# Kernel optimization log

Measured on AMD Instinct MI355X. Metric: run time of the kernel, lower is better.

The kernel has to match this reference:

```python
import jax, jax.numpy as jnp
import numpy as np

B, T, N, IN, H, P = 1, 48, 4096, 2, 64, 12


def _normalize_adj(adj):
    A = adj + jnp.eye(adj.shape[0], dtype=adj.dtype)
    d = jnp.sum(A, axis=1)
    dinv = jnp.where(d > 0, d ** -0.5, 0.0)
    return (dinv[:, None] * A) * dinv[None, :]


def _cell(inp, h, c, A, gcWi, gcbi, gcWh, gcbh, liWi, libi, liWh, libh):
    # graph conv: spmm(A, inp @ W) + bias, plus plain linears; all produce [BN, 4H]
    comb = (A @ (inp @ gcWi) + gcbi
            + A @ (h @ gcWh) + gcbh
            + inp @ liWi + libi
            + h @ liWh + libh)
    i_g, f_g, o_g, g_g = jnp.split(comb, 4, axis=1)
    new_c = jax.nn.sigmoid(f_g) * c + jax.nn.sigmoid(i_g) * jnp.tanh(g_g)
    new_h = jax.nn.sigmoid(o_g) * jnp.tanh(new_c)
    return new_h, new_c


def setup_inputs() -> dict:
    key = jax.random.key(0)
    ks = jax.random.split(key, 24)
    s_in = 1.0 / np.sqrt(4 * H)

    def p(k, shape):
        return jax.random.normal(k, shape, dtype=jnp.float32) * s_in

    adj = (jax.random.uniform(ks[1], (N, N)) < 0.01).astype(jnp.float32)
    return {
        "x": jax.random.normal(ks[0], (B, T, N * IN), dtype=jnp.float32),
        "adj": adj,
        "gcWi0": p(ks[2], (IN, 4 * H)), "gcbi0": p(ks[3], (4 * H,)),
        "gcWh0": p(ks[4], (H, 4 * H)), "gcbh0": p(ks[5], (4 * H,)),
        "liWi0": p(ks[6], (IN, 4 * H)), "libi0": p(ks[7], (4 * H,)),
        "liWh0": p(ks[8], (H, 4 * H)), "libh0": p(ks[9], (4 * H,)),
        "gcWi1": p(ks[10], (H, 4 * H)), "gcbi1": p(ks[11], (4 * H,)),
        "gcWh1": p(ks[12], (H, 4 * H)), "gcbh1": p(ks[13], (4 * H,)),
        "liWi1": p(ks[14], (H, 4 * H)), "libi1": p(ks[15], (4 * H,)),
        "liWh1": p(ks[16], (H, 4 * H)), "libh1": p(ks[17], (4 * H,)),
        "outW": p(ks[18], (H, P)), "outb": p(ks[19], (P,)),
    }


def reference(x, adj, gcWi0, gcbi0, gcWh0, gcbh0, liWi0, libi0, liWh0, libh0,
              gcWi1, gcbi1, gcWh1, gcbh1, liWi1, libi1, liWh1, libh1, outW, outb):
    A = _normalize_adj(adj)
    # [B,T,N*IN] -> time-major [T, B*N, IN]
    xs = x.reshape(B, T, N, IN).transpose(1, 0, 2, 3).reshape(T, B * N, IN)
    z = jnp.zeros((B * N, H), dtype=x.dtype)

    def step(carry, xt):
        h0, c0, h1, c1 = carry
        h0, c0 = _cell(xt, h0, c0, A, gcWi0, gcbi0, gcWh0, gcbh0,
                       liWi0, libi0, liWh0, libh0)
        # dropout is identity in eval mode
        h1, c1 = _cell(h0, h1, c1, A, gcWi1, gcbi1, gcWh1, gcbh1,
                       liWi1, libi1, liWh1, libh1)
        return (h0, c0, h1, c1), None

    (h0, c0, h1, c1), _ = jax.lax.scan(step, (z, z, z, z), xs)
    out = h1 @ outW + outb  # [B*N, P]
    return out.reshape(B, N, P)
```

## Files before the change

### kernel.cpp

```cpp
#include <hip/hip_runtime.h>
#include <math.h>

#define NN 4096
#define TT 48
#define HH 64
#define GG 256
#define PP 12
#define CAP 192
#define NH (NN * HH)

__device__ __forceinline__ float bcast_f(float v, int lane) {
  return __int_as_float(__builtin_amdgcn_readlane(__float_as_int(v), lane));
}
__device__ __forceinline__ int bcast_i(int v, int lane) {
  return __builtin_amdgcn_readlane(v, lane);
}

__launch_bounds__(256)
__global__ void k_prep(const float* gcbi0, const float* gcbh0,
                       const float* libi0, const float* libh0,
                       const float* gcbi1, const float* gcbh1,
                       const float* libi1, const float* libh1,
                       const float* gcWh0, const float* liWh0,
                       const float* gcWi1, const float* liWi1,
                       const float* gcWh1, const float* liWh1,
                       const float* gcWi0, const float* liWi0,
                       float* state, float4* Wg0, float4* Wg1,
                       float4* biasg0, float4* biasg1, float4* xq0) {
  int idx = blockIdx.x * 256 + threadIdx.x;
  int stride = gridDim.x * 256;
  for (int i = idx; i < 6 * NH; i += stride) state[i] = 0.0f;
  for (int i = idx; i < 64 * 2 * 64; i += stride) {
    int j = i & 63, m = (i >> 6) & 1, k = i >> 7;
    const float* W = m ? liWh0 : gcWh0;
    Wg0[i] = make_float4(W[k * GG + j], W[k * GG + j + 64],
                         W[k * GG + j + 128], W[k * GG + j + 192]);
  }
  for (int i = idx; i < 64 * 4 * 64; i += stride) {
    int j = i & 63, m = (i >> 6) & 3, k = i >> 8;
    const float* W = (m == 0) ? gcWi1 : (m == 1) ? liWi1 : (m == 2) ? gcWh1 : liWh1;
    Wg1[i] = make_float4(W[k * GG + j], W[k * GG + j + 64],
                         W[k * GG + j + 128], W[k * GG + j + 192]);
  }
  if (idx < 64) {
    int j = idx;
    biasg0[j] = make_float4(
        gcbi0[j] + gcbh0[j] + libi0[j] + libh0[j],
        gcbi0[j + 64] + gcbh0[j + 64] + libi0[j + 64] + libh0[j + 64],
        gcbi0[j + 128] + gcbh0[j + 128] + libi0[j + 128] + libh0[j + 128],
        gcbi0[j + 192] + gcbh0[j + 192] + libi0[j + 192] + libh0[j + 192]);
    biasg1[j] = make_float4(
        gcbi1[j] + gcbh1[j] + libi1[j] + libh1[j],
        gcbi1[j + 64] + gcbh1[j + 64] + libi1[j + 64] + libh1[j + 64],
        gcbi1[j + 128] + gcbh1[j + 128] + libi1[j + 128] + libh1[j + 128],
        gcbi1[j + 192] + gcbh1[j + 192] + libi1[j + 192] + libh1[j + 192]);
  } else if (idx < 320) {
    int i = idx - 64;
    int j = i & 63, m = i >> 6;
    const float* W = (m < 2) ? gcWi0 : liWi0;
    int kk = m & 1;
    xq0[i] = make_float4(W[kk * GG + j], W[kk * GG + j + 64],
                         W[kk * GG + j + 128], W[kk * GG + j + 192]);
  }
}

__launch_bounds__(256)
__global__ void k_build(const float* adj, float* dinv,
                        int* ell_col, float* ell_val, int* ell_cnt) {
  int r = blockIdx.x;
  __shared__ int cnt;
  __shared__ float red[256];
  if (threadIdx.x == 0) cnt = 0;
  __syncthreads();
  const float* row = adj + (size_t)r * NN;
  float s = 0.0f;
  for (int c = threadIdx.x; c < NN; c += 256) {
    float a = row[c];
    if (c == r) a += 1.0f;
    s += a;
    if (a != 0.0f) {
      int pos = atomicAdd(&cnt, 1);
      if (pos < CAP) {
        ell_col[(size_t)r * CAP + pos] = c;
        ell_val[(size_t)r * CAP + pos] = a;
      }
    }
  }
  red[threadIdx.x] = s;
  __syncthreads();
  for (int st = 128; st > 0; st >>= 1) {
    if (threadIdx.x < st) red[threadIdx.x] += red[threadIdx.x + st];
    __syncthreads();
  }
  int n = cnt < CAP ? cnt : CAP;
  for (int j = n + (int)threadIdx.x; j < CAP; j += 256) {
    ell_col[(size_t)r * CAP + j] = 0;
    ell_val[(size_t)r * CAP + j] = 0.0f;
  }
  if (threadIdx.x == 0) {
    int npad = (n + 7) & ~7;
    if (npad > CAP) npad = CAP;
    ell_cnt[r] = npad;
    dinv[r] = 1.0f / sqrtf(red[0]);
  }
}

__launch_bounds__(256)
__global__ void k_scale(const float* dinv, const int* ell_col, float* ell_val) {
  int idx = blockIdx.x * 256 + threadIdx.x;
  int r = idx / CAP;
  if (r >= NN) return;
  float v = ell_val[idx];
  if (v != 0.0f) ell_val[idx] = v * dinv[r] * dinv[ell_col[idx]];
}

__launch_bounds__(256)
__global__ void k_gax(const float* x, const int* ell_col, const float* ell_val,
                      const int* ell_cnt, float* gax) {
  int t = blockIdx.x >> 3;
  int seg = blockIdx.x & 7;
  __shared__ float xs[NN * 2];
  const float* xt = x + (size_t)t * NN * 2;
  for (int i = threadIdx.x; i < NN * 2; i += 256) xs[i] = xt[i];
  __syncthreads();
  int base = seg * 512 * 2;
  for (int oo = threadIdx.x; oo < 512 * 2; oo += 256) {
    int o = base + oo;
    int r = o >> 1, cmp = o & 1;
    int cnt = ell_cnt[r];
    const int* cp = ell_col + (size_t)r * CAP;
    const float* vp = ell_val + (size_t)r * CAP;
    float acc = 0.0f;
    for (int j = 0; j < cnt; j += 4) {
      acc += vp[j]     * xs[cp[j]     * 2 + cmp];
      acc += vp[j + 1] * xs[cp[j + 1] * 2 + cmp];
      acc += vp[j + 2] * xs[cp[j + 2] * 2 + cmp];
      acc += vp[j + 3] * xs[cp[j + 3] * 2 + cmp];
    }
    gax[(size_t)t * NN * 2 + o] = acc;
  }
}

__device__ __forceinline__ void cell0_body(
    int blk,
    const int* __restrict__ ell_col, const float* __restrict__ ell_val,
    const int* __restrict__ ell_cnt,
    const float2* __restrict__ Pr, float* __restrict__ Pw,
    float* __restrict__ c0,
    const float* __restrict__ xt, const float* __restrict__ gaxt,
    const float4* __restrict__ Wg0, const float4* __restrict__ biasg0,
    const float4* __restrict__ xq0) {
  const int tid = threadIdx.x;
  const int wave = tid >> 6, lane = tid & 63;
  const int r0 = blk * 8 + wave * 2;

  int myc[2][3]; float myv[2][3]; int cnts[2];
#pragma unroll
  for (int rr = 0; rr < 2; rr++) {
    int r = r0 + rr;
    cnts[rr] = ell_cnt[r];
#pragma unroll
    for (int chk = 0; chk < 3; chk++) {
      myc[rr][chk] = ell_col[(size_t)r * CAP + chk * 64 + lane];
      myv[rr][chk] = ell_val[(size_t)r * CAP + chk * 64 + lane];
    }
  }
  float gacc[2], hl[2];
#pragma unroll
  for (int rr = 0; rr < 2; rr++) {
    int cnt = cnts[rr];
    float acc = 0.0f;
#pragma unroll
    for (int chk = 0; chk < 3; chk++) {
      int base = chk * 64;
      if (base < cnt) {
        int lim = cnt - base; if (lim > 64) lim = 64;
        int mc = myc[rr][chk]; float mv = myv[rr][chk];
        for (int m = 0; m < lim; m += 8) {
          float2 ld[8]; float vv[8];
#pragma unroll
          for (int i = 0; i < 8; i++) {
            int cc = bcast_i(mc, m + i);
            vv[i] = bcast_f(mv, m + i);
            ld[i] = Pr[(size_t)cc * 64 + lane];
          }
#pragma unroll
          for (int i = 0; i < 8; i++) acc += vv[i] * ld[i].x;
        }
      }
    }
    gacc[rr] = acc;
    hl[rr] = Pr[(size_t)(r0 + rr) * 64 + lane].x;
  }

  float4 acc[2];
  {
    float4 b = biasg0[lane];
    float4 qg0 = xq0[lane], qg1 = xq0[64 + lane];
    float4 ql0 = xq0[128 + lane], ql1 = xq0[192 + lane];
#pragma unroll
    for (int rr = 0; rr < 2; rr++) {
      float xx0 = xt[(size_t)(r0 + rr) * 2];
      float xx1 = xt[(size_t)(r0 + rr) * 2 + 1];
      float gg0 = gaxt[(size_t)(r0 + rr) * 2];
      float gg1 = gaxt[(size_t)(r0 + rr) * 2 + 1];
      acc[rr].x = b.x + gg0 * qg0.x + gg1 * qg1.x + xx0 * ql0.x + xx1 * ql1.x;
      acc[rr].y = b.y + gg0 * qg0.y + gg1 * qg1.y + xx0 * ql0.y + xx1 * ql1.y;
      acc[rr].z = b.z + gg0 * qg0.z + gg1 * qg1.z + xx0 * ql0.z + xx1 * ql1.z;
      acc[rr].w = b.w + gg0 * qg0.w + gg1 * qg1.w + xx0 * ql0.w + xx1 * ql1.w;
    }
  }

  const float4* bw = Wg0 + lane;
#pragma unroll 4
  for (int k = 0; k < 64; k++) {
    float4 w0 = bw[(k * 2 + 0) * 64];
    float4 w1 = bw[(k * 2 + 1) * 64];
#pragma unroll
    for (int rr = 0; rr < 2; rr++) {
      float a0 = bcast_f(gacc[rr], k);
      float a1 = bcast_f(hl[rr], k);
      acc[rr].x += a0 * w0.x + a1 * w1.x;
      acc[rr].y += a0 * w0.y + a1 * w1.y;
      acc[rr].z += a0 * w0.z + a1 * w1.z;
      acc[rr].w += a0 * w0.w + a1 * w1.w;
    }
  }

#pragma unroll
  for (int rr = 0; rr < 2; rr++) {
    size_t gi = (size_t)(r0 + rr) * HH + lane;
    float cprev = c0[gi];
    float si = 1.0f / (1.0f + __expf(-acc[rr].x));
    float sf = 1.0f / (1.0f + __expf(-acc[rr].y));
    float so = 1.0f / (1.0f + __expf(-acc[rr].z));
    float cn = sf * cprev + si * tanhf(acc[rr].w);
    float hn = so * tanhf(cn);
    c0[gi] = cn;
    Pw[gi * 2 + 0] = hn;
  }
}

__device__ __forceinline__ void cell1_body(
    int blk,
    const int* __restrict__ ell_col, const float* __restrict__ ell_val,
    const int* __restrict__ ell_cnt,
    const float2* __restrict__ Pr, float* __restrict__ Pw,
    float* __restrict__ c1,
    const float4* __restrict__ Wg1, const float4* __restrict__ biasg1) {
  const int tid = threadIdx.x;
  const int wave = tid >> 6, lane = tid & 63;
  const int r0 = blk * 8 + wave * 2;

  int myc[2][3]; float myv[2][3]; int cnts[2];
#pragma unroll
  for (int rr = 0; rr < 2; rr++) {
    int r = r0 + rr;
    cnts[rr] = ell_cnt[r];
#pragma unroll
    for (int chk = 0; chk < 3; chk++) {
      myc[rr][chk] = ell_col[(size_t)r * CAP + chk * 64 + lane];
      myv[rr][chk] = ell_val[(size_t)r * CAP + chk * 64 + lane];
    }
  }
  float ga0[2], ga1[2], hl0[2], hl1[2];
#pragma unroll
  for (int rr = 0; rr < 2; rr++) {
    int cnt = cnts[rr];
    float a0 = 0.0f, a1 = 0.0f;
#pragma unroll
    for (int chk = 0; chk < 3; chk++) {
      int base = chk * 64;
      if (base < cnt) {
        int lim = cnt - base; if (lim > 64) lim = 64;
        int mc = myc[rr][chk]; float mv = myv[rr][chk];
        for (int m = 0; m < lim; m += 8) {
          float2 ld[8]; float vv[8];
#pragma unroll
          for (int i = 0; i < 8; i++) {
            int cc = bcast_i(mc, m + i);
            vv[i] = bcast_f(mv, m + i);
            ld[i] = Pr[(size_t)cc * 64 + lane];
          }
#pragma unroll
          for (int i = 0; i < 8; i++) {
            a0 += vv[i] * ld[i].x;
            a1 += vv[i] * ld[i].y;
          }
        }
      }
    }
    ga0[rr] = a0;
    ga1[rr] = a1;
    float2 hh = Pr[(size_t)(r0 + rr) * 64 + lane];
    hl0[rr] = hh.x;
    hl1[rr] = hh.y;
  }

  float4 acc[2];
  {
    float4 b = biasg1[lane];
    acc[0] = b; acc[1] = b;
  }
  const float4* bw = Wg1 + lane;
#pragma unroll 4
  for (int k = 0; k < 64; k++) {
    float4 w0 = bw[(k * 4 + 0) * 64];
    float4 w1 = bw[(k * 4 + 1) * 64];
    float4 w2 = bw[(k * 4 + 2) * 64];
    float4 w3 = bw[(k * 4 + 3) * 64];
#pragma unroll
    for (int rr = 0; rr < 2; rr++) {
      float a0 = bcast_f(ga0[rr], k);
      float a1 = bcast_f(hl0[rr], k);
      float a2 = bcast_f(ga1[rr], k);
      float a3 = bcast_f(hl1[rr], k);
      acc[rr].x += a0 * w0.x + a1 * w1.x + a2 * w2.x + a3 * w3.x;
      acc[rr].y += a0 * w0.y + a1 * w1.y + a2 * w2.y + a3 * w3.y;
      acc[rr].z += a0 * w0.z + a1 * w1.z + a2 * w2.z + a3 * w3.z;
      acc[rr].w += a0 * w0.w + a1 * w1.w + a2 * w2.w + a3 * w3.w;
    }
  }

#pragma unroll
  for (int rr = 0; rr < 2; rr++) {
    size_t gi = (size_t)(r0 + rr) * HH + lane;
    float cprev = c1[gi];
    float si = 1.0f / (1.0f + __expf(-acc[rr].x));
    float sf = 1.0f / (1.0f + __expf(-acc[rr].y));
    float so = 1.0f / (1.0f + __expf(-acc[rr].z));
    float cn = sf * cprev + si * tanhf(acc[rr].w);
    float hn = so * tanhf(cn);
    c1[gi] = cn;
    Pw[gi * 2 + 1] = hn;
  }
}

__launch_bounds__(256)
__global__ void k_cells(int c0blocks,
                        const int* __restrict__ ell_col,
                        const float* __restrict__ ell_val,
                        const int* __restrict__ ell_cnt,
                        const float2* __restrict__ Pr, float* __restrict__ Pw,
                        float* __restrict__ c0, float* __restrict__ c1,
                        const float* __restrict__ xt, const float* __restrict__ gaxt,
                        const float4* __restrict__ Wg0,
                        const float4* __restrict__ biasg0,
                        const float4* __restrict__ xq0,
                        const float4* __restrict__ Wg1,
                        const float4* __restrict__ biasg1) {
  int b = blockIdx.x;
  if (b < c0blocks) {
    cell0_body(b, ell_col, ell_val, ell_cnt, Pr, Pw, c0, xt, gaxt,
               Wg0, biasg0, xq0);
  } else {
    cell1_body(b - c0blocks, ell_col, ell_val, ell_cnt, Pr, Pw, c1,
               Wg1, biasg1);
  }
}

__launch_bounds__(256)
__global__ void k_out(const float* __restrict__ P0, const float* __restrict__ outW,
                      const float* __restrict__ outb, float* __restrict__ out) {
  int idx = blockIdx.x * 256 + threadIdx.x;
  if (idx >= NN * PP) return;
  int r = idx / PP, p = idx - r * PP;
  float acc = outb[p];
  const float* hrow = P0 + (size_t)r * 128;
#pragma unroll 16
  for (int k = 0; k < HH; k++) acc += hrow[k * 2 + 1] * outW[k * PP + p];
  out[idx] = acc;
}

extern "C" void kernel_launch(void* const* d_in, const int* in_sizes, int n_in,
                              void* d_out, int out_size, void* d_ws, size_t ws_size,
                              hipStream_t stream) {
  const float* x     = (const float*)d_in[0];
  const float* adj   = (const float*)d_in[1];
  const float* gcWi0 = (const float*)d_in[2];
  const float* gcbi0 = (const float*)d_in[3];
  const float* gcWh0 = (const float*)d_in[4];
  const float* gcbh0 = (const float*)d_in[5];
  const float* liWi0 = (const float*)d_in[6];
  const float* libi0 = (const float*)d_in[7];
  const float* liWh0 = (const float*)d_in[8];
  const float* libh0 = (const float*)d_in[9];
  const float* gcWi1 = (const float*)d_in[10];
  const float* gcbi1 = (const float*)d_in[11];
  const float* gcWh1 = (const float*)d_in[12];
  const float* gcbh1 = (const float*)d_in[13];
  const float* liWi1 = (const float*)d_in[14];
  const float* libi1 = (const float*)d_in[15];
  const float* liWh1 = (const float*)d_in[16];
  const float* libh1 = (const float*)d_in[17];
  const float* outW  = (const float*)d_in[18];
  const float* outb  = (const float*)d_in[19];

  char* ws = (char*)d_ws;
  size_t off = 0;
  auto carve = [&](size_t bytes) {
    void* p = ws + off;
    off += (bytes + 255) & ~(size_t)255;
    return p;
  };
  float*  dinv    = (float*)carve((size_t)NN * 4);
  int*    ell_col = (int*)carve((size_t)NN * CAP * 4);
  float*  ell_val = (float*)carve((size_t)NN * CAP * 4);
  int*    ell_cnt = (int*)carve((size_t)NN * 4);
  float*  state   = (float*)carve((size_t)6 * NH * 4);
  float*  gax     = (float*)carve((size_t)TT * NN * 2 * 4);
  float4* Wg0     = (float4*)carve((size_t)64 * 2 * 64 * 16);
  float4* Wg1     = (float4*)carve((size_t)64 * 4 * 64 * 16);
  float4* biasg0  = (float4*)carve((size_t)64 * 16);
  float4* biasg1  = (float4*)carve((size_t)64 * 16);
  float4* xq0     = (float4*)carve((size_t)256 * 16);

  float* P[2] = {state, state + 2 * NH};
  float* c0 = state + 4 * NH;
  float* c1 = state + 5 * NH;

  k_prep<<<512, 256, 0, stream>>>(gcbi0, gcbh0, libi0, libh0,
                                  gcbi1, gcbh1, libi1, libh1,
                                  gcWh0, liWh0, gcWi1, liWi1, gcWh1, liWh1,
                                  gcWi0, liWi0,
                                  state, Wg0, Wg1, biasg0, biasg1, xq0);
  k_build<<<NN, 256, 0, stream>>>(adj, dinv, ell_col, ell_val, ell_cnt);
  k_scale<<<(NN * CAP) / 256, 256, 0, stream>>>(dinv, ell_col, ell_val);
  k_gax<<<TT * 8, 256, 0, stream>>>(x, ell_col, ell_val, ell_cnt, gax);

  for (int k = 0; k <= TT; k++) {
    int A = k & 1;
    int c0blocks = (k < TT) ? NN / 8 : 0;
    int c1blocks = (k > 0) ? NN / 8 : 0;
    int grid = c0blocks + c1blocks;
    int tx = (k < TT) ? k : (TT - 1);
    k_cells<<<grid, 256, 0, stream>>>(
        c0blocks, ell_col, ell_val, ell_cnt,
        (const float2*)P[A ^ 1], P[A], c0, c1,
        x + (size_t)tx * NN * 2, gax + (size_t)tx * NN * 2,
        Wg0, biasg0, xq0, Wg1, biasg1);
  }

  k_out<<<(NN * PP + 255) / 256, 256, 0, stream>>>(P[0], outW, outb, (float*)d_out);
}
```

Before: 2.080 ms.

## Split dense gate matmul across waves by K-slices with shared-memory reduction

Each block now stages its 8 rows of aggregated activations and hidden state in shared memory. Each wave then handles a 16-wide K slice for all 8 rows instead of the full K range for 2 rows, so every wave loads only a quarter of the weight matrix per block. Partial sums are reduced through shared memory by wave 0, which then applies the LSTM gates. This cuts redundant weight loads, at the cost of two block barriers, about 30KB of LDS per block, a serialized epilogue on one wave, and a launch bound hint of 4 blocks per CU.

```diff
diff --git a/kernel.cpp b/kernel.cpp
--- a/kernel.cpp
+++ b/kernel.cpp
@@ -141,8 +141,10 @@
   }
 }
 
+#define ASTR 65
+
 __device__ __forceinline__ void cell0_body(
-    int blk,
+    int blk, float* actS, float4* redS,
     const int* __restrict__ ell_col, const float* __restrict__ ell_val,
     const int* __restrict__ ell_cnt,
     const float2* __restrict__ Pr, float* __restrict__ Pw,
@@ -152,30 +154,21 @@
     const float4* __restrict__ xq0) {
   const int tid = threadIdx.x;
   const int wave = tid >> 6, lane = tid & 63;
-  const int r0 = blk * 8 + wave * 2;
-
-  int myc[2][3]; float myv[2][3]; int cnts[2];
+  const int r0 = blk * 8;
+
 #pragma unroll
   for (int rr = 0; rr < 2; rr++) {
-    int r = r0 + rr;
-    cnts[rr] = ell_cnt[r];
-#pragma unroll
-    for (int chk = 0; chk < 3; chk++) {
-      myc[rr][chk] = ell_col[(size_t)r * CAP + chk * 64 + lane];
-      myv[rr][chk] = ell_val[(size_t)r * CAP + chk * 64 + lane];
-    }
-  }
-  float gacc[2], hl[2];
-#pragma unroll
-  for (int rr = 0; rr < 2; rr++) {
-    int cnt = cnts[rr];
+    int rloc = 2 * wave + rr;
+    int r = r0 + rloc;
+    int cnt = ell_cnt[r];
     float acc = 0.0f;
 #pragma unroll
     for (int chk = 0; chk < 3; chk++) {
       int base = chk * 64;
       if (base < cnt) {
         int lim = cnt - base; if (lim > 64) lim = 64;
-        int mc = myc[rr][chk]; float mv = myv[rr][chk];
+        int mc = ell_col[(size_t)r * CAP + base + lane];
+        float mv = ell_val[(size_t)r * CAP + base + lane];
         for (int m = 0; m < lim; m += 8) {
           float2 ld[8]; float vv[8];
 #pragma unroll
@@ -189,60 +182,86 @@
         }
       }
     }
-    gacc[rr] = acc;
-    hl[rr] = Pr[(size_t)(r0 + rr) * 64 + lane].x;
-  }
-
-  float4 acc[2];
-  {
+    actS[(rloc * 2 + 0) * ASTR + lane] = acc;
+    actS[(rloc * 2 + 1) * ASTR + lane] = Pr[(size_t)r * 64 + lane].x;
+  }
+  __syncthreads();
+
+  const int kk0 = wave * 16;
+  const int lm = lane & 1, lk = (lane >> 1) & 15;
+  float areg[8];
+#pragma unroll
+  for (int r = 0; r < 8; r++)
+    areg[r] = actS[(r * 2 + lm) * ASTR + kk0 + lk];
+
+  float4 acc[8];
+  if (wave == 0) {
     float4 b = biasg0[lane];
     float4 qg0 = xq0[lane], qg1 = xq0[64 + lane];
     float4 ql0 = xq0[128 + lane], ql1 = xq0[192 + lane];
 #pragma unroll
-    for (int rr = 0; rr < 2; rr++) {
-      float xx0 = xt[(size_t)(r0 + rr) * 2];
-      float xx1 = xt[(size_t)(r0 + rr) * 2 + 1];
-      float gg0 = gaxt[(size_t)(r0 + rr) * 2];
-      float gg1 = gaxt[(size_t)(r0 + rr) * 2 + 1];
-      acc[rr].x = b.x + gg0 * qg0.x + gg1 * qg1.x + xx0 * ql0.x + xx1 * ql1.x;
-      acc[rr].y = b.y + gg0 * qg0.y + gg1 * qg1.y + xx0 * ql0.y + xx1 * ql1.y;
-      acc[rr].z = b.z + gg0 * qg0.z + gg1 * qg1.z + xx0 * ql0.z + xx1 * ql1.z;
-      acc[rr].w = b.w + gg0 * qg0.w + gg1 * qg1.w + xx0 * ql0.w + xx1 * ql1.w;
-    }
+    for (int r = 0; r < 8; r++) {
+      float xx0 = xt[(size_t)(r0 + r) * 2];
+      float xx1 = xt[(size_t)(r0 + r) * 2 + 1];
+      float gg0 = gaxt[(size_t)(r0 + r) * 2];
+      float gg1 = gaxt[(size_t)(r0 + r) * 2 + 1];
+      acc[r].x = b.x + gg0 * qg0.x + gg1 * qg1.x + xx0 * ql0.x + xx1 * ql1.x;
+      acc[r].y = b.y + gg0 * qg0.y + gg1 * qg1.y + xx0 * ql0.y + xx1 * ql1.y;
+      acc[r].z = b.z + gg0 * qg0.z + gg1 * qg1.z + xx0 * ql0.z + xx1 * ql1.z;
+      acc[r].w = b.w + gg0 * qg0.w + gg1 * qg1.w + xx0 * ql0.w + xx1 * ql1.w;
+    }
+  } else {
+#pragma unroll
+    for (int r = 0; r < 8; r++) acc[r] = make_float4(0.f, 0.f, 0.f, 0.f);
   }
 
   const float4* bw = Wg0 + lane;
-#pragma unroll 4
-  for (int k = 0; k < 64; k++) {
+#pragma unroll
+  for (int kk = 0; kk < 16; kk++) {
+    int k = kk0 + kk;
     float4 w0 = bw[(k * 2 + 0) * 64];
     float4 w1 = bw[(k * 2 + 1) * 64];
 #pragma unroll
-    for (int rr = 0; rr < 2; rr++) {
-      float a0 = bcast_f(gacc[rr], k);
-      float a1 = bcast_f(hl[rr], k);
-      acc[rr].x += a0 * w0.x + a1 * w1.x;
-      acc[rr].y += a0 * w0.y + a1 * w1.y;
-      acc[rr].z += a0 * w0.z + a1 * w1.z;
-      acc[rr].w += a0 * w0.w + a1 * w1.w;
-    }
-  }
-
-#pragma unroll
-  for (int rr = 0; rr < 2; rr++) {
-    size_t gi = (size_t)(r0 + rr) * HH + lane;
-    float cprev = c0[gi];
-    float si = 1.0f / (1.0f + __expf(-acc[rr].x));
-    float sf = 1.0f / (1.0f + __expf(-acc[rr].y));
-    float so = 1.0f / (1.0f + __expf(-acc[rr].z));
-    float cn = sf * cprev + si * tanhf(acc[rr].w);
-    float hn = so * tanhf(cn);
-    c0[gi] = cn;
-    Pw[gi * 2 + 0] = hn;
+    for (int r = 0; r < 8; r++) {
+      float a0 = bcast_f(areg[r], kk * 2 + 0);
+      float a1 = bcast_f(areg[r], kk * 2 + 1);
+      acc[r].x += a0 * w0.x + a1 * w1.x;
+      acc[r].y += a0 * w0.y + a1 * w1.y;
+      acc[r].z += a0 * w0.z + a1 * w1.z;
+      acc[r].w += a0 * w0.w + a1 * w1.w;
+    }
+  }
+
+  if (wave > 0) {
+#pragma unroll
+    for (int r = 0; r < 8; r++)
+      redS[(wave - 1) * 512 + r * 64 + lane] = acc[r];
+  }
+  __syncthreads();
+  if (wave == 0) {
+#pragma unroll
+    for (int r = 0; r < 8; r++) {
+      float4 t = acc[r];
+#pragma unroll
+      for (int w = 0; w < 3; w++) {
+        float4 p = redS[w * 512 + r * 64 + lane];
+        t.x += p.x; t.y += p.y; t.z += p.z; t.w += p.w;
+      }
+      size_t gi = (size_t)(r0 + r) * HH + lane;
+      float cprev = c0[gi];
+      float si = 1.0f / (1.0f + __expf(-t.x));
+      float sf = 1.0f / (1.0f + __expf(-t.y));
+      float so = 1.0f / (1.0f + __expf(-t.z));
+      float cn = sf * cprev + si * tanhf(t.w);
+      float hn = so * tanhf(cn);
+      c0[gi] = cn;
+      Pw[gi * 2 + 0] = hn;
+    }
   }
 }
 
 __device__ __forceinline__ void cell1_body(
-    int blk,
+    int blk, float* actS, float4* redS,
     const int* __restrict__ ell_col, const float* __restrict__ ell_val,
     const int* __restrict__ ell_cnt,
     const float2* __restrict__ Pr, float* __restrict__ Pw,
@@ -250,30 +269,21 @@
     const float4* __restrict__ Wg1, const float4* __restrict__ biasg1) {
   const int tid = threadIdx.x;
   const int wave = tid >> 6, lane = tid & 63;
-  const int r0 = blk * 8 + wave * 2;
-
-  int myc[2][3]; float myv[2][3]; int cnts[2];
+  const int r0 = blk * 8;
+
 #pragma unroll
   for (int rr = 0; rr < 2; rr++) {
-    int r = r0 + rr;
-    cnts[rr] = ell_cnt[r];
-#pragma unroll
-    for (int chk = 0; chk < 3; chk++) {
-      myc[rr][chk] = ell_col[(size_t)r * CAP + chk * 64 + lane];
-      myv[rr][chk] = ell_val[(size_t)r * CAP + chk * 64 + lane];
-    }
-  }
-  float ga0[2], ga1[2], hl0[2], hl1[2];
-#pragma unroll
-  for (int rr = 0; rr < 2; rr++) {
-    int cnt = cnts[rr];
+    int rloc = 2 * wave + rr;
+    int r = r0 + rloc;
+    int cnt = ell_cnt[r];
     float a0 = 0.0f, a1 = 0.0f;
 #pragma unroll
     for (int chk = 0; chk < 3; chk++) {
       int base = chk * 64;
       if (base < cnt) {
         int lim = cnt - base; if (lim > 64) lim = 64;
-        int mc = myc[rr][chk]; float mv = myv[rr][chk];
+        int mc = ell_col[(size_t)r * CAP + base + lane];
+        float mv = ell_val[(size_t)r * CAP + base + lane];
         for (int m = 0; m < lim; m += 8) {
           float2 ld[8]; float vv[8];
 #pragma unroll
@@ -290,53 +300,81 @@
         }
       }
     }
-    ga0[rr] = a0;
-    ga1[rr] = a1;
-    float2 hh = Pr[(size_t)(r0 + rr) * 64 + lane];
-    hl0[rr] = hh.x;
-    hl1[rr] = hh.y;
-  }
-
-  float4 acc[2];
-  {
+    float2 hh = Pr[(size_t)r * 64 + lane];
+    actS[(rloc * 4 + 0) * ASTR + lane] = a0;
+    actS[(rloc * 4 + 1) * ASTR + lane] = hh.x;
+    actS[(rloc * 4 + 2) * ASTR + lane] = a1;
+    actS[(rloc * 4 + 3) * ASTR + lane] = hh.y;
+  }
+  __syncthreads();
+
+  const int kk0 = wave * 16;
+  const int lm = lane & 3, lk = lane >> 2;
+  float areg[8];
+#pragma unroll
+  for (int r = 0; r < 8; r++)
+    areg[r] = actS[(r * 4 + lm) * ASTR + kk0 + lk];
+
+  float4 acc[8];
+  if (wave == 0) {
     float4 b = biasg1[lane];
-    acc[0] = b; acc[1] = b;
-  }
+#pragma unroll
+    for (int r = 0; r < 8; r++) acc[r] = b;
+  } else {
+#pragma unroll
+    for (int r = 0; r < 8; r++) acc[r] = make_float4(0.f, 0.f, 0.f, 0.f);
+  }
+
   const float4* bw = Wg1 + lane;
-#pragma unroll 4
-  for (int k = 0; k < 64; k++) {
+#pragma unroll
+  for (int kk = 0; kk < 16; kk++) {
+    int k = kk0 + kk;
     float4 w0 = bw[(k * 4 + 0) * 64];
     float4 w1 = bw[(k * 4 + 1) * 64];
     float4 w2 = bw[(k * 4 + 2) * 64];
     float4 w3 = bw[(k * 4 + 3) * 64];
 #pragma unroll
-    for (int rr = 0; rr < 2; rr++) {
-      float a0 = bcast_f(ga0[rr], k);
-      float a1 = bcast_f(hl0[rr], k);
-      float a2 = bcast_f(ga1[rr], k);
-      float a3 = bcast_f(hl1[rr], k);
-      acc[rr].x += a0 * w0.x + a1 * w1.x + a2 * w2.x + a3 * w3.x;
-      acc[rr].y += a0 * w0.y + a1 * w1.y + a2 * w2.y + a3 * w3.y;
-      acc[rr].z += a0 * w0.z + a1 * w1.z + a2 * w2.z + a3 * w3.z;
-      acc[rr].w += a0 * w0.w + a1 * w1.w + a2 * w2.w + a3 * w3.w;
-    }
-  }
-
-#pragma unroll
-  for (int rr = 0; rr < 2; rr++) {
-    size_t gi = (size_t)(r0 + rr) * HH + lane;
-    float cprev = c1[gi];
-    float si = 1.0f / (1.0f + __expf(-acc[rr].x));
-    float sf = 1.0f / (1.0f + __expf(-acc[rr].y));
-    float so = 1.0f / (1.0f + __expf(-acc[rr].z));
-    float cn = sf * cprev + si * tanhf(acc[rr].w);
-    float hn = so * tanhf(cn);
-    c1[gi] = cn;
-    Pw[gi * 2 + 1] = hn;
-  }
-}
-
-__launch_bounds__(256)
+    for (int r = 0; r < 8; r++) {
+      float a0 = bcast_f(areg[r], kk * 4 + 0);
+      float a1 = bcast_f(areg[r], kk * 4 + 1);
+      float a2 = bcast_f(areg[r], kk * 4 + 2);
+      float a3 = bcast_f(areg[r], kk * 4 + 3);
+      acc[r].x += a0 * w0.x + a1 * w1.x + a2 * w2.x + a3 * w3.x;
+      acc[r].y += a0 * w0.y + a1 * w1.y + a2 * w2.y + a3 * w3.y;
+      acc[r].z += a0 * w0.z + a1 * w1.z + a2 * w2.z + a3 * w3.z;
+      acc[r].w += a0 * w0.w + a1 * w1.w + a2 * w2.w + a3 * w3.w;
+    }
+  }
+
+  if (wave > 0) {
+#pragma unroll
+    for (int r = 0; r < 8; r++)
+      redS[(wave - 1) * 512 + r * 64 + lane] = acc[r];
+  }
+  __syncthreads();
+  if (wave == 0) {
+#pragma unroll
+    for (int r = 0; r < 8; r++) {
+      float4 t = acc[r];
+#pragma unroll
+      for (int w = 0; w < 3; w++) {
+        float4 p = redS[w * 512 + r * 64 + lane];
+        t.x += p.x; t.y += p.y; t.z += p.z; t.w += p.w;
+      }
+      size_t gi = (size_t)(r0 + r) * HH + lane;
+      float cprev = c1[gi];
+      float si = 1.0f / (1.0f + __expf(-t.x));
+      float sf = 1.0f / (1.0f + __expf(-t.y));
+      float so = 1.0f / (1.0f + __expf(-t.z));
+      float cn = sf * cprev + si * tanhf(t.w);
+      float hn = so * tanhf(cn);
+      c1[gi] = cn;
+      Pw[gi * 2 + 1] = hn;
+    }
+  }
+}
+
+__launch_bounds__(256, 4)
 __global__ void k_cells(int c0blocks,
                         const int* __restrict__ ell_col,
                         const float* __restrict__ ell_val,
@@ -349,12 +387,14 @@
                         const float4* __restrict__ xq0,
                         const float4* __restrict__ Wg1,
                         const float4* __restrict__ biasg1) {
+  __shared__ float actS[8 * 4 * ASTR];
+  __shared__ float4 redS[3 * 512];
   int b = blockIdx.x;
   if (b < c0blocks) {
-    cell0_body(b, ell_col, ell_val, ell_cnt, Pr, Pw, c0, xt, gaxt,
-               Wg0, biasg0, xq0);
+    cell0_body(b, actS, redS, ell_col, ell_val, ell_cnt, Pr, Pw, c0,
+               xt, gaxt, Wg0, biasg0, xq0);
   } else {
-    cell1_body(b - c0blocks, ell_col, ell_val, ell_cnt, Pr, Pw, c1,
+    cell1_body(b - c0blocks, actS, redS, ell_col, ell_val, ell_cnt, Pr, Pw, c1,
                Wg1, biasg1);
   }
 }
```

After: 6.175 ms. +196.9%, slower.
